# Performance work log

Hardware: AMD Instinct MI355X
Metric: run time of the kernel (lower is better)

## Reference

```python
import jax, jax.numpy as jnp
import numpy as np

B, S, D, E, K, FF = 4, 2048, 1024, 8, 2, 4096  # batch, seq, d_model, experts, top-k, 4*d_model


def setup_inputs() -> dict:
    key = jax.random.key(0)
    k0, k1, k2, k3 = jax.random.split(key, 4)
    scale = 0.02
    return {
        "x": jax.random.normal(k0, (B, S, D), jnp.float32),
        "gate_w": jax.random.normal(k1, (D, E), jnp.float32) * scale,
        "w1": jax.random.normal(k2, (E, D, FF), jnp.float32) * scale,
        "b1": jnp.zeros((E, FF), jnp.float32),
        "w2": jax.random.normal(k3, (E, FF, D), jnp.float32) * scale,
        "b2": jnp.zeros((E, D), jnp.float32),
    }


def reference(x, gate_w, w1, b1, w2, b2):
    # Gating: top-k logits, softmax over the selected k (matches torch.topk + softmax)
    logits = jnp.einsum("bsd,de->bse", x, gate_w)  # [B,S,E]
    vals, idxs = jax.lax.top_k(logits, K)           # [B,S,K]
    w = jax.nn.softmax(vals, axis=-1)               # [B,S,K]
    n_exp = gate_w.shape[-1]
    # Per-token combine weight for each expert (0 if not selected)
    combine = jnp.sum(jax.nn.one_hot(idxs, n_exp, dtype=x.dtype) * w[..., None], axis=-2)  # [B,S,E]

    out = jnp.zeros_like(x)
    for e in range(n_exp):  # fixed small loop over experts
        h = jax.nn.silu(jnp.einsum("bsd,df->bsf", x, w1[e]) + b1[e])  # dropout = identity (eval)
        y = jnp.einsum("bsf,fd->bsd", h, w2[e]) + b2[e]
        out = out + combine[..., e:e + 1] * y
    return out
```

## Files before the change

kernel.cpp:

```cpp
#include <hip/hip_runtime.h>
#include <math.h>

#define Tt 8192
#define Dd 1024
#define Ee 8
#define FFf 4096
#define SLOTS (Tt*2)

typedef unsigned short u16;
typedef unsigned int u32;
typedef __attribute__((ext_vector_type(8))) __bf16 bf16x8;
typedef __attribute__((ext_vector_type(4))) float f32x4;

__device__ __forceinline__ u16 f2bf(float f) {
  union { float f; u32 u; } v; v.f = f;
  u32 u = v.u;
  return (u16)((u + 0x7FFFu + ((u >> 16) & 1u)) >> 16);
}
__device__ __forceinline__ float bf2f(u16 h) {
  union { u32 u; float f; } v; v.u = ((u32)h) << 16; return v.f;
}
__device__ __forceinline__ void gl2lds16(const u16* g, u16* l) {
  __builtin_amdgcn_global_load_lds((const __attribute__((address_space(1))) void*)g,
                                   (__attribute__((address_space(3))) void*)l, 16, 0, 0);
}

__global__ void gate_topk_kernel(const float* __restrict__ x,
                                 const float* __restrict__ gw,
                                 int* __restrict__ counts,
                                 int* __restrict__ tok_e,
                                 float* __restrict__ tok_w,
                                 u16* __restrict__ xb) {
  int wave = (int)((blockIdx.x * blockDim.x + threadIdx.x) >> 6);
  int lane = threadIdx.x & 63;
  if (wave >= Tt) return;
  const float* xrow = x + (size_t)wave * Dd;
  int d0 = lane * 16;
  const f32x4* xr4 = (const f32x4*)(xrow + d0);
  f32x4 v0 = xr4[0], v1 = xr4[1], v2 = xr4[2], v3 = xr4[3];
  float xv[16];
#pragma unroll
  for (int k = 0; k < 4; k++) { xv[k] = v0[k]; xv[4 + k] = v1[k]; xv[8 + k] = v2[k]; xv[12 + k] = v3[k]; }
  float p[Ee];
#pragma unroll
  for (int e = 0; e < Ee; e++) p[e] = 0.f;
#pragma unroll
  for (int i = 0; i < 16; i++) {
    const float* g = gw + (size_t)(d0 + i) * Ee;
#pragma unroll
    for (int e = 0; e < Ee; e++) p[e] += xv[i] * g[e];
  }
  {
    uint4 o0, o1;
    o0.x = (u32)f2bf(xv[0]) | ((u32)f2bf(xv[1]) << 16);
    o0.y = (u32)f2bf(xv[2]) | ((u32)f2bf(xv[3]) << 16);
    o0.z = (u32)f2bf(xv[4]) | ((u32)f2bf(xv[5]) << 16);
    o0.w = (u32)f2bf(xv[6]) | ((u32)f2bf(xv[7]) << 16);
    o1.x = (u32)f2bf(xv[8]) | ((u32)f2bf(xv[9]) << 16);
    o1.y = (u32)f2bf(xv[10]) | ((u32)f2bf(xv[11]) << 16);
    o1.z = (u32)f2bf(xv[12]) | ((u32)f2bf(xv[13]) << 16);
    o1.w = (u32)f2bf(xv[14]) | ((u32)f2bf(xv[15]) << 16);
    u16* dp = xb + (size_t)wave * Dd + d0;
    *(uint4*)dp = o0;
    *(uint4*)(dp + 8) = o1;
  }
#pragma unroll
  for (int e = 0; e < Ee; e++) {
    for (int off = 32; off > 0; off >>= 1) p[e] += __shfl_xor(p[e], off, 64);
  }
  if (lane == 0) {
    int e0 = 0; float v0s = p[0];
#pragma unroll
    for (int e = 1; e < Ee; e++) if (p[e] > v0s) { v0s = p[e]; e0 = e; }
    int e1 = -1; float v1s = -INFINITY;
#pragma unroll
    for (int e = 0; e < Ee; e++) if (e != e0 && p[e] > v1s) { v1s = p[e]; e1 = e; }
    float w0 = 1.f / (1.f + expf(v1s - v0s));
    float w1 = 1.f - w0;
    tok_e[wave * 2 + 0] = e0; tok_e[wave * 2 + 1] = e1;
    tok_w[wave * 2 + 0] = w0; tok_w[wave * 2 + 1] = w1;
    atomicAdd(&counts[e0], 1);
    atomicAdd(&counts[e1], 1);
  }
}

__global__ __launch_bounds__(256) void wconv_kernel(const float* __restrict__ src,
                                                    u16* __restrict__ dst, int R, int C) {
  __shared__ float t[64][65];
  int e = blockIdx.z;
  size_t ebase = (size_t)e * R * C;
  int r0 = blockIdx.y * 64, c0 = blockIdx.x * 64;
  int tid = threadIdx.x;
  int row = tid >> 2, q = tid & 3;
  const float* sp = src + ebase + (size_t)(r0 + row) * C + c0 + q * 16;
  f32x4 v0 = *(const f32x4*)(sp);
  f32x4 v1 = *(const f32x4*)(sp + 4);
  f32x4 v2 = *(const f32x4*)(sp + 8);
  f32x4 v3 = *(const f32x4*)(sp + 12);
#pragma unroll
  for (int k = 0; k < 4; k++) t[row][q * 16 + k] = v0[k];
#pragma unroll
  for (int k = 0; k < 4; k++) t[row][q * 16 + 4 + k] = v1[k];
#pragma unroll
  for (int k = 0; k < 4; k++) t[row][q * 16 + 8 + k] = v2[k];
#pragma unroll
  for (int k = 0; k < 4; k++) t[row][q * 16 + 12 + k] = v3[k];
  __syncthreads();
  float c[16];
#pragma unroll
  for (int k = 0; k < 16; k++) c[k] = t[q * 16 + k][row];
  uint4 d0, d1;
  d0.x = (u32)f2bf(c[0]) | ((u32)f2bf(c[1]) << 16);
  d0.y = (u32)f2bf(c[2]) | ((u32)f2bf(c[3]) << 16);
  d0.z = (u32)f2bf(c[4]) | ((u32)f2bf(c[5]) << 16);
  d0.w = (u32)f2bf(c[6]) | ((u32)f2bf(c[7]) << 16);
  d1.x = (u32)f2bf(c[8]) | ((u32)f2bf(c[9]) << 16);
  d1.y = (u32)f2bf(c[10]) | ((u32)f2bf(c[11]) << 16);
  d1.z = (u32)f2bf(c[12]) | ((u32)f2bf(c[13]) << 16);
  d1.w = (u32)f2bf(c[14]) | ((u32)f2bf(c[15]) << 16);
  u16* dp = dst + ebase + (size_t)(c0 + row) * R + r0 + q * 16;
  *(uint4*)dp = d0;
  *(uint4*)(dp + 8) = d1;
}

__global__ void scan_kernel(const int* __restrict__ counts,
                            int* __restrict__ offsets, int* __restrict__ cursors) {
  if (threadIdx.x == 0 && blockIdx.x == 0) {
    int acc = 0;
    for (int e = 0; e < Ee; e++) { offsets[e] = acc; cursors[e] = acc; acc += counts[e]; }
  }
}

__global__ void scatter_kernel(const int* __restrict__ tok_e, const float* __restrict__ tok_w,
                               int* __restrict__ cursors,
                               int* __restrict__ slot_token, float* __restrict__ slot_w,
                               int* __restrict__ tok_slot) {
  int t = blockIdx.x * blockDim.x + threadIdx.x;
  if (t >= Tt) return;
#pragma unroll
  for (int k = 0; k < 2; k++) {
    int e = tok_e[t * 2 + k];
    int pos = atomicAdd(&cursors[e], 1);
    slot_token[pos] = t;
    slot_w[pos] = tok_w[t * 2 + k];
    tok_slot[t * 2 + k] = pos;
  }
}

#define MFMA16(H)                                                                 \
  do {                                                                            \
    acc[H][0][0] = __builtin_amdgcn_mfma_f32_16x16x32_bf16(a0, b0, acc[H][0][0], 0, 0, 0); \
    acc[H][0][1] = __builtin_amdgcn_mfma_f32_16x16x32_bf16(a0, b1, acc[H][0][1], 0, 0, 0); \
    acc[H][0][2] = __builtin_amdgcn_mfma_f32_16x16x32_bf16(a0, b2, acc[H][0][2], 0, 0, 0); \
    acc[H][0][3] = __builtin_amdgcn_mfma_f32_16x16x32_bf16(a0, b3, acc[H][0][3], 0, 0, 0); \
    acc[H][1][0] = __builtin_amdgcn_mfma_f32_16x16x32_bf16(a1, b0, acc[H][1][0], 0, 0, 0); \
    acc[H][1][1] = __builtin_amdgcn_mfma_f32_16x16x32_bf16(a1, b1, acc[H][1][1], 0, 0, 0); \
    acc[H][1][2] = __builtin_amdgcn_mfma_f32_16x16x32_bf16(a1, b2, acc[H][1][2], 0, 0, 0); \
    acc[H][1][3] = __builtin_amdgcn_mfma_f32_16x16x32_bf16(a1, b3, acc[H][1][3], 0, 0, 0); \
    acc[H][2][0] = __builtin_amdgcn_mfma_f32_16x16x32_bf16(a2, b0, acc[H][2][0], 0, 0, 0); \
    acc[H][2][1] = __builtin_amdgcn_mfma_f32_16x16x32_bf16(a2, b1, acc[H][2][1], 0, 0, 0); \
    acc[H][2][2] = __builtin_amdgcn_mfma_f32_16x16x32_bf16(a2, b2, acc[H][2][2], 0, 0, 0); \
    acc[H][2][3] = __builtin_amdgcn_mfma_f32_16x16x32_bf16(a2, b3, acc[H][2][3], 0, 0, 0); \
    acc[H][3][0] = __builtin_amdgcn_mfma_f32_16x16x32_bf16(a3, b0, acc[H][3][0], 0, 0, 0); \
    acc[H][3][1] = __builtin_amdgcn_mfma_f32_16x16x32_bf16(a3, b1, acc[H][3][1], 0, 0, 0); \
    acc[H][3][2] = __builtin_amdgcn_mfma_f32_16x16x32_bf16(a3, b2, acc[H][3][2], 0, 0, 0); \
    acc[H][3][3] = __builtin_amdgcn_mfma_f32_16x16x32_bf16(a3, b3, acc[H][3][3], 0, 0, 0); \
  } while (0)

template<int KDIM, int NDIM, int EPI, int GATHER, int NT>
__device__ __forceinline__ void moe_body(
    const u16* __restrict__ A, const u16* __restrict__ BT,
    const float* __restrict__ bias,
    const int* __restrict__ offsets, const int* __restrict__ counts,
    const int* __restrict__ slot_token, const float* __restrict__ slot_w,
    u16* __restrict__ O16, float* __restrict__ Of,
    int rb, int kbase) {
  int e = blockIdx.z;
  int cnt = counts[e];
  if (rb * 256 >= cnt) return;
  int off = offsets[e];
  int n0 = blockIdx.x * 256;

  __shared__ u16 S[65536];

  int tid = threadIdx.x;
  int lane = tid & 63, wave = tid >> 6;
  int wr = wave >> 2, wc = wave & 3;
  int lr = lane & 15, g = lane >> 4;

  const u16* BTe = BT + (size_t)e * NDIM * KDIM;

  const u16* aSrc[2][2];
  const u16* bSrc[2][2];
  int amax = off + cnt - 1;
#pragma unroll
  for (int h = 0; h < 2; h++)
#pragma unroll
    for (int s = 0; s < 2; s++) {
      int c = tid + s * 512;
      int lc = c ^ (((c >> 5) & 1) << 1);
      int ks = lc >> 9, rl = (lc >> 2) & 127, seg = lc & 3;
      int slotRow = off + rb * 256 + h * 128 + rl;
      if (slotRow > amax) slotRow = amax;
      int arow = GATHER ? slot_token[slotRow] : slotRow;
      aSrc[h][s] = A + (size_t)arow * KDIM + kbase + ks * 32 + seg * 8;
    }
#pragma unroll
  for (int ks = 0; ks < 2; ks++)
#pragma unroll
    for (int s = 0; s < 2; s++) {
      int c = tid + s * 512;
      int lc = c ^ (((c >> 5) & 1) << 1);
      int row = lc >> 2, seg = lc & 3;
      bSrc[ks][s] = BTe + (size_t)(n0 + row) * KDIM + kbase + ks * 32 + seg * 8;
    }

  auto stA = [&](int u, int h) {
    u16* d = &S[(u & 1) * 16384 + h * 8192 + wave * 512];
    gl2lds16(aSrc[h][0] + (size_t)u * 64, d);
    gl2lds16(aSrc[h][1] + (size_t)u * 64, d + 4096);
  };
  auto stB = [&](int u, int ks) {
    u16* d = &S[32768 + (u & 1) * 16384 + ks * 8192 + wave * 512];
    gl2lds16(bSrc[ks][0] + (size_t)u * 64, d);
    gl2lds16(bSrc[ks][1] + (size_t)u * 64, d + 4096);
  };
  auto rdA = [&](int dbuf, int hm, int ks, int i) -> bf16x8 {
    int rl = wr * 64 + i * 16 + lr;
    int logb = ks * 8192 + rl * 64 + g * 16;
    int phys = logb ^ (((rl >> 3) & 1) << 5);
    return *reinterpret_cast<const bf16x8*>(&S[dbuf * 16384 + hm * 8192 + (phys >> 1)]);
  };
  auto rdB = [&](int dbuf, int ks, int j) -> bf16x8 {
    int row = wc * 64 + j * 16 + lr;
    int logb = row * 64 + g * 16;
    int phys = logb ^ (((row >> 3) & 1) << 5);
    return *reinterpret_cast<const bf16x8*>(&S[32768 + dbuf * 16384 + ks * 8192 + (phys >> 1)]);
  };

  f32x4 acc[2][4][4];
#pragma unroll
  for (int h = 0; h < 2; h++)
#pragma unroll
    for (int i = 0; i < 4; i++)
#pragma unroll
      for (int j = 0; j < 4; j++) acc[h][i][j] = (f32x4)(0.0f);

  stB(0, 0); stA(0, 0); stA(0, 1); stB(0, 1);
  stB(1, 0); stA(1, 0);
  asm volatile("s_waitcnt vmcnt(4)" ::: "memory");
  __builtin_amdgcn_s_barrier();

  bf16x8 b0, b1, b2, b3;
  for (int t = 0; t < NT; ++t) {
    int dbuf = t & 1;
    {
      bf16x8 a0 = rdA(dbuf, 0, 0, 0), a1 = rdA(dbuf, 0, 0, 1),
             a2 = rdA(dbuf, 0, 0, 2), a3 = rdA(dbuf, 0, 0, 3);
      b0 = rdB(dbuf, 0, 0); b1 = rdB(dbuf, 0, 1); b2 = rdB(dbuf, 0, 2); b3 = rdB(dbuf, 0, 3);
      if (t + 1 < NT) stA(t + 1, 1);
      __builtin_amdgcn_s_barrier();
      asm volatile("s_waitcnt lgkmcnt(0)" ::: "memory");
      __builtin_amdgcn_sched_barrier(0);
      __builtin_amdgcn_s_setprio(1);
      MFMA16(0);
      __builtin_amdgcn_s_setprio(0);
      __builtin_amdgcn_s_barrier();
    }
    {
      bf16x8 a0 = rdA(dbuf, 1, 0, 0), a1 = rdA(dbuf, 1, 0, 1),
             a2 = rdA(dbuf, 1, 0, 2), a3 = rdA(dbuf, 1, 0, 3);
      if (t + 1 < NT) {
        stB(t + 1, 1);
        asm volatile("s_waitcnt vmcnt(6)" ::: "memory");
      }
      __builtin_amdgcn_s_barrier();
      asm volatile("s_waitcnt lgkmcnt(0)" ::: "memory");
      __builtin_amdgcn_sched_barrier(0);
      __builtin_amdgcn_s_setprio(1);
      MFMA16(1);
      __builtin_amdgcn_s_setprio(0);
      __builtin_amdgcn_s_barrier();
    }
    {
      bf16x8 a0 = rdA(dbuf, 0, 1, 0), a1 = rdA(dbuf, 0, 1, 1),
             a2 = rdA(dbuf, 0, 1, 2), a3 = rdA(dbuf, 0, 1, 3);
      b0 = rdB(dbuf, 1, 0); b1 = rdB(dbuf, 1, 1); b2 = rdB(dbuf, 1, 2); b3 = rdB(dbuf, 1, 3);
      if (t + 2 < NT) stB(t + 2, 0);
      __builtin_amdgcn_s_barrier();
      asm volatile("s_waitcnt lgkmcnt(0)" ::: "memory");
      __builtin_amdgcn_sched_barrier(0);
      __builtin_amdgcn_s_setprio(1);
      MFMA16(0);
      __builtin_amdgcn_s_setprio(0);
      __builtin_amdgcn_s_barrier();
    }
    {
      bf16x8 a0 = rdA(dbuf, 1, 1, 0), a1 = rdA(dbuf, 1, 1, 1),
             a2 = rdA(dbuf, 1, 1, 2), a3 = rdA(dbuf, 1, 1, 3);
      if (t + 2 < NT) {
        stA(t + 2, 0);
        asm volatile("s_waitcnt vmcnt(6)" ::: "memory");
      } else if (t + 1 < NT) {
        asm volatile("s_waitcnt vmcnt(0)" ::: "memory");
      }
      __builtin_amdgcn_s_barrier();
      asm volatile("s_waitcnt lgkmcnt(0)" ::: "memory");
      __builtin_amdgcn_sched_barrier(0);
      __builtin_amdgcn_s_setprio(1);
      MFMA16(1);
      __builtin_amdgcn_s_setprio(0);
      __builtin_amdgcn_s_barrier();
    }
  }

  int rlim = cnt - rb * 256;
#pragma unroll
  for (int hm = 0; hm < 2; hm++)
#pragma unroll
    for (int i = 0; i < 4; i++)
#pragma unroll
      for (int q = 0; q < 4; q++) {
        int m = hm * 128 + wr * 64 + i * 16 + g * 4 + q;
        if (m < rlim) {
          int slot = off + rb * 256 + m;
#pragma unroll
          for (int j = 0; j < 4; j++) {
            int n = n0 + wc * 64 + j * 16 + lr;
            float v = acc[hm][i][j][q];
            if (bias != nullptr) v += bias[e * NDIM + n];
            if (EPI == 0) {
              float sv = v / (1.f + expf(-v));
              O16[(size_t)slot * NDIM + n] = f2bf(sv);
            } else if (EPI == 1) {
              O16[(size_t)slot * NDIM + n] = f2bf(v * slot_w[slot]);
            } else {
              atomicAdd(Of + (size_t)slot_token[slot] * NDIM + n, v * slot_w[slot]);
            }
          }
        }
      }
}

__global__ __launch_bounds__(512, 2) void moe_g1_kernel(
    const u16* __restrict__ A, const u16* __restrict__ BT, const float* __restrict__ bias,
    const int* __restrict__ offsets, const int* __restrict__ counts,
    const int* __restrict__ slot_token, const float* __restrict__ slot_w,
    u16* __restrict__ O16) {
  moe_body<Dd, FFf, 0, 1, Dd / 64>(A, BT, bias, offsets, counts, slot_token, slot_w,
                                   O16, nullptr, blockIdx.y, 0);
}
__global__ __launch_bounds__(512, 2) void moe_g2s_kernel(
    const u16* __restrict__ A, const u16* __restrict__ BT, const float* __restrict__ bias,
    const int* __restrict__ offsets, const int* __restrict__ counts,
    const int* __restrict__ slot_token, const float* __restrict__ slot_w,
    u16* __restrict__ y) {
  int ksp = blockIdx.y & 1;
  moe_body<FFf, Dd, 1, 0, FFf / 128>(A, BT, ksp ? nullptr : bias, offsets, counts,
                                     slot_token, slot_w,
                                     y + (size_t)ksp * SLOTS * Dd, nullptr,
                                     blockIdx.y >> 1, ksp * (FFf / 2));
}
__global__ __launch_bounds__(512, 2) void moe_g2_kernel(
    const u16* __restrict__ A, const u16* __restrict__ BT, const float* __restrict__ bias,
    const int* __restrict__ offsets, const int* __restrict__ counts,
    const int* __restrict__ slot_token, const float* __restrict__ slot_w,
    u16* __restrict__ O16) {
  moe_body<FFf, Dd, 1, 0, FFf / 64>(A, BT, bias, offsets, counts, slot_token, slot_w,
                                    O16, nullptr, blockIdx.y, 0);
}
__global__ __launch_bounds__(512, 2) void moe_g2_atomic_kernel(
    const u16* __restrict__ A, const u16* __restrict__ BT, const float* __restrict__ bias,
    const int* __restrict__ offsets, const int* __restrict__ counts,
    const int* __restrict__ slot_token, const float* __restrict__ slot_w,
    float* __restrict__ Of) {
  moe_body<FFf, Dd, 2, 0, FFf / 64>(A, BT, bias, offsets, counts, slot_token, slot_w,
                                    nullptr, Of, blockIdx.y, 0);
}

__global__ void combine_kernel(const u16* __restrict__ y, const int* __restrict__ tok_slot,
                               float* __restrict__ out) {
  int gid = blockIdx.x * blockDim.x + threadIdx.x;
  int t = gid >> 7;
  int seg = gid & 127;
  int s0 = tok_slot[t * 2 + 0], s1 = tok_slot[t * 2 + 1];
  uint4 a = *(const uint4*)(y + (size_t)s0 * Dd + seg * 8);
  uint4 b = *(const uint4*)(y + (size_t)s1 * Dd + seg * 8);
  f32x4 o0, o1;
  o0[0] = bf2f((u16)a.x) + bf2f((u16)b.x);
  o0[1] = bf2f((u16)(a.x >> 16)) + bf2f((u16)(b.x >> 16));
  o0[2] = bf2f((u16)a.y) + bf2f((u16)b.y);
  o0[3] = bf2f((u16)(a.y >> 16)) + bf2f((u16)(b.y >> 16));
  o1[0] = bf2f((u16)a.z) + bf2f((u16)b.z);
  o1[1] = bf2f((u16)(a.z >> 16)) + bf2f((u16)(b.z >> 16));
  o1[2] = bf2f((u16)a.w) + bf2f((u16)b.w);
  o1[3] = bf2f((u16)(a.w >> 16)) + bf2f((u16)(b.w >> 16));
  float* op = out + (size_t)t * Dd + seg * 8;
  *(f32x4*)op = o0;
  *(f32x4*)(op + 4) = o1;
}

__global__ void combine4_kernel(const u16* __restrict__ y, const int* __restrict__ tok_slot,
                                float* __restrict__ out) {
  int gid = blockIdx.x * blockDim.x + threadIdx.x;
  int t = gid >> 7;
  int seg = gid & 127;
  int s0 = tok_slot[t * 2 + 0], s1 = tok_slot[t * 2 + 1];
  const u16* y1 = y + (size_t)SLOTS * Dd;
  uint4 a = *(const uint4*)(y  + (size_t)s0 * Dd + seg * 8);
  uint4 b = *(const uint4*)(y1 + (size_t)s0 * Dd + seg * 8);
  uint4 c = *(const uint4*)(y  + (size_t)s1 * Dd + seg * 8);
  uint4 d = *(const uint4*)(y1 + (size_t)s1 * Dd + seg * 8);
  f32x4 o0, o1;
  o0[0] = bf2f((u16)a.x) + bf2f((u16)b.x) + bf2f((u16)c.x) + bf2f((u16)d.x);
  o0[1] = bf2f((u16)(a.x >> 16)) + bf2f((u16)(b.x >> 16)) + bf2f((u16)(c.x >> 16)) + bf2f((u16)(d.x >> 16));
  o0[2] = bf2f((u16)a.y) + bf2f((u16)b.y) + bf2f((u16)c.y) + bf2f((u16)d.y);
  o0[3] = bf2f((u16)(a.y >> 16)) + bf2f((u16)(b.y >> 16)) + bf2f((u16)(c.y >> 16)) + bf2f((u16)(d.y >> 16));
  o1[0] = bf2f((u16)a.z) + bf2f((u16)b.z) + bf2f((u16)c.z) + bf2f((u16)d.z);
  o1[1] = bf2f((u16)(a.z >> 16)) + bf2f((u16)(b.z >> 16)) + bf2f((u16)(c.z >> 16)) + bf2f((u16)(d.z >> 16));
  o1[2] = bf2f((u16)a.w) + bf2f((u16)b.w) + bf2f((u16)c.w) + bf2f((u16)d.w);
  o1[3] = bf2f((u16)(a.w >> 16)) + bf2f((u16)(b.w >> 16)) + bf2f((u16)(c.w >> 16)) + bf2f((u16)(d.w >> 16));
  float* op = out + (size_t)t * Dd + seg * 8;
  *(f32x4*)op = o0;
  *(f32x4*)(op + 4) = o1;
}

extern "C" void kernel_launch(void* const* d_in, const int* in_sizes, int n_in,
                              void* d_out, int out_size, void* d_ws, size_t ws_size,
                              hipStream_t stream) {
  const float* x  = (const float*)d_in[0];
  const float* gw = (const float*)d_in[1];
  const float* w1 = (const float*)d_in[2];
  const float* b1 = (const float*)d_in[3];
  const float* w2 = (const float*)d_in[4];
  const float* b2 = (const float*)d_in[5];
  float* out = (float*)d_out;

  char* ws = (char*)d_ws;
  size_t off_counts = 0;
  size_t off_offsets = 256;
  size_t off_cursors = 512;
  size_t off_tok_e = 1024;
  size_t off_tok_w     = off_tok_e + (size_t)Tt * 2 * 4;
  size_t off_tok_slot  = off_tok_w + (size_t)Tt * 2 * 4;
  size_t off_slot_token= off_tok_slot + (size_t)Tt * 2 * 4;
  size_t off_slot_w    = off_slot_token + (size_t)SLOTS * 4;
  size_t off_xb        = off_slot_w + (size_t)SLOTS * 4;
  size_t off_h         = off_xb + (size_t)Tt * Dd * 2;
  size_t off_wT        = off_h + (size_t)SLOTS * FFf * 2;
  size_t off_y         = off_wT + (size_t)Ee * Dd * FFf * 2;
  size_t need_atomic   = off_y;
  size_t need_y1       = off_y + (size_t)SLOTS * Dd * 2;
  size_t need_y2       = off_y + (size_t)SLOTS * Dd * 2 * 2;
  if (ws_size < need_atomic) return;
  int tier = (ws_size >= need_y2) ? 2 : (ws_size >= need_y1) ? 1 : 0;

  int* counts     = (int*)(ws + off_counts);
  int* offsets    = (int*)(ws + off_offsets);
  int* cursors    = (int*)(ws + off_cursors);
  int* tok_e      = (int*)(ws + off_tok_e);
  float* tok_w    = (float*)(ws + off_tok_w);
  int* tok_slot   = (int*)(ws + off_tok_slot);
  int* slot_token = (int*)(ws + off_slot_token);
  float* slot_w   = (float*)(ws + off_slot_w);
  u16* xb         = (u16*)(ws + off_xb);
  u16* h          = (u16*)(ws + off_h);
  u16* wT         = (u16*)(ws + off_wT);
  u16* y          = (u16*)(ws + off_y);

  hipMemsetAsync(ws, 0, 1024, stream);

  gate_topk_kernel<<<Tt / 4, 256, 0, stream>>>(x, gw, counts, tok_e, tok_w, xb);
  scan_kernel<<<1, 64, 0, stream>>>(counts, offsets, cursors);
  scatter_kernel<<<Tt / 256, 256, 0, stream>>>(tok_e, tok_w, cursors, slot_token, slot_w, tok_slot);

  {
    dim3 gc(FFf / 64, Dd / 64, Ee);
    wconv_kernel<<<gc, 256, 0, stream>>>(w1, wT, Dd, FFf);
  }
  {
    dim3 g1(FFf / 256, Tt / 256, Ee);
    moe_g1_kernel<<<g1, 512, 0, stream>>>(xb, wT, b1, offsets, counts,
                                          slot_token, slot_w, h);
  }
  {
    dim3 gc(Dd / 64, FFf / 64, Ee);
    wconv_kernel<<<gc, 256, 0, stream>>>(w2, wT, FFf, Dd);
  }
  if (tier == 2) {
    dim3 g2(Dd / 256, (Tt / 256) * 2, Ee);
    moe_g2s_kernel<<<g2, 512, 0, stream>>>(h, wT, b2, offsets, counts,
                                           slot_token, slot_w, y);
    combine4_kernel<<<(Tt * 128) / 256, 256, 0, stream>>>(y, tok_slot, out);
  } else if (tier == 1) {
    dim3 g2(Dd / 256, Tt / 256, Ee);
    moe_g2_kernel<<<g2, 512, 0, stream>>>(h, wT, b2, offsets, counts,
                                          slot_token, slot_w, y);
    combine_kernel<<<(Tt * 128) / 256, 256, 0, stream>>>(y, tok_slot, out);
  } else {
    hipMemsetAsync(d_out, 0, (size_t)out_size * sizeof(float), stream);
    dim3 g2(Dd / 256, Tt / 256, Ee);
    moe_g2_atomic_kernel<<<g2, 512, 0, stream>>>(h, wT, b2, offsets, counts,
                                                 slot_token, slot_w, out);
  }
}
```

Before: 848.5 us.

## Fold scan into gating kernel, recoalesce weight transpose, unroll GEMM loop

The single-thread scan kernel is removed and its offsets/cursors computation is done by the last block of the gating kernel, detected with a done counter and threadfence. The weight transpose-and-convert kernel is reorganised so each thread loads one float4 per row and writes 8-element bf16 chunks, giving more coalesced global access. The main GEMM K-loop gets an unroll-by-2 pragma. These save a kernel launch and aim to speed up weight conversion, at the cost of an extra atomic per block and possibly higher register use in the GEMM.

```diff
diff --git a/kernel.cpp b/kernel.cpp
--- a/kernel.cpp
+++ b/kernel.cpp
@@ -30,10 +30,12 @@
                                  int* __restrict__ counts,
                                  int* __restrict__ tok_e,
                                  float* __restrict__ tok_w,
-                                 u16* __restrict__ xb) {
+                                 u16* __restrict__ xb,
+                                 int* __restrict__ offsets,
+                                 int* __restrict__ cursors,
+                                 int* __restrict__ done) {
   int wave = (int)((blockIdx.x * blockDim.x + threadIdx.x) >> 6);
   int lane = threadIdx.x & 63;
-  if (wave >= Tt) return;
   const float* xrow = x + (size_t)wave * Dd;
   int d0 = lane * 16;
   const f32x4* xr4 = (const f32x4*)(xrow + d0);
@@ -82,6 +84,15 @@
     atomicAdd(&counts[e0], 1);
     atomicAdd(&counts[e1], 1);
   }
+  __syncthreads();
+  if (threadIdx.x == 0) {
+    __threadfence();
+    int t = atomicAdd(done, 1);
+    if (t == (int)gridDim.x - 1) {
+      int acc = 0;
+      for (int e = 0; e < Ee; e++) { offsets[e] = acc; cursors[e] = acc; acc += counts[e]; }
+    }
+  }
 }
 
 __global__ __launch_bounds__(256) void wconv_kernel(const float* __restrict__ src,
@@ -91,43 +102,29 @@
   size_t ebase = (size_t)e * R * C;
   int r0 = blockIdx.y * 64, c0 = blockIdx.x * 64;
   int tid = threadIdx.x;
-  int row = tid >> 2, q = tid & 3;
-  const float* sp = src + ebase + (size_t)(r0 + row) * C + c0 + q * 16;
-  f32x4 v0 = *(const f32x4*)(sp);
-  f32x4 v1 = *(const f32x4*)(sp + 4);
-  f32x4 v2 = *(const f32x4*)(sp + 8);
-  f32x4 v3 = *(const f32x4*)(sp + 12);
-#pragma unroll
-  for (int k = 0; k < 4; k++) t[row][q * 16 + k] = v0[k];
-#pragma unroll
-  for (int k = 0; k < 4; k++) t[row][q * 16 + 4 + k] = v1[k];
-#pragma unroll
-  for (int k = 0; k < 4; k++) t[row][q * 16 + 8 + k] = v2[k];
-#pragma unroll
-  for (int k = 0; k < 4; k++) t[row][q * 16 + 12 + k] = v3[k];
+  int rr = tid >> 4;
+  int cc = (tid & 15) * 4;
+#pragma unroll
+  for (int p = 0; p < 4; p++) {
+    int row = rr + p * 16;
+    f32x4 v = *(const f32x4*)(src + ebase + (size_t)(r0 + row) * C + c0 + cc);
+    t[row][cc] = v[0]; t[row][cc + 1] = v[1]; t[row][cc + 2] = v[2]; t[row][cc + 3] = v[3];
+  }
   __syncthreads();
-  float c[16];
-#pragma unroll
-  for (int k = 0; k < 16; k++) c[k] = t[q * 16 + k][row];
-  uint4 d0, d1;
-  d0.x = (u32)f2bf(c[0]) | ((u32)f2bf(c[1]) << 16);
-  d0.y = (u32)f2bf(c[2]) | ((u32)f2bf(c[3]) << 16);
-  d0.z = (u32)f2bf(c[4]) | ((u32)f2bf(c[5]) << 16);
-  d0.w = (u32)f2bf(c[6]) | ((u32)f2bf(c[7]) << 16);
-  d1.x = (u32)f2bf(c[8]) | ((u32)f2bf(c[9]) << 16);
-  d1.y = (u32)f2bf(c[10]) | ((u32)f2bf(c[11]) << 16);
-  d1.z = (u32)f2bf(c[12]) | ((u32)f2bf(c[13]) << 16);
-  d1.w = (u32)f2bf(c[14]) | ((u32)f2bf(c[15]) << 16);
-  u16* dp = dst + ebase + (size_t)(c0 + row) * R + r0 + q * 16;
-  *(uint4*)dp = d0;
-  *(uint4*)(dp + 8) = d1;
-}
-
-__global__ void scan_kernel(const int* __restrict__ counts,
-                            int* __restrict__ offsets, int* __restrict__ cursors) {
-  if (threadIdx.x == 0 && blockIdx.x == 0) {
-    int acc = 0;
-    for (int e = 0; e < Ee; e++) { offsets[e] = acc; cursors[e] = acc; acc += counts[e]; }
+  int c = tid >> 3;
+  int rseg = (tid & 7) * 8;
+#pragma unroll
+  for (int p = 0; p < 2; p++) {
+    int cp = c + p * 32;
+    float f[8];
+#pragma unroll
+    for (int i = 0; i < 8; i++) f[i] = t[rseg + i][cp];
+    uint4 o;
+    o.x = (u32)f2bf(f[0]) | ((u32)f2bf(f[1]) << 16);
+    o.y = (u32)f2bf(f[2]) | ((u32)f2bf(f[3]) << 16);
+    o.z = (u32)f2bf(f[4]) | ((u32)f2bf(f[5]) << 16);
+    o.w = (u32)f2bf(f[6]) | ((u32)f2bf(f[7]) << 16);
+    *(uint4*)(dst + ebase + (size_t)(c0 + cp) * R + r0 + rseg) = o;
   }
 }
 
@@ -252,6 +249,7 @@
   __builtin_amdgcn_s_barrier();
 
   bf16x8 b0, b1, b2, b3;
+#pragma unroll 2
   for (int t = 0; t < NT; ++t) {
     int dbuf = t & 1;
     {
@@ -359,7 +357,7 @@
   moe_body<FFf, Dd, 1, 0, FFf / 128>(A, BT, ksp ? nullptr : bias, offsets, counts,
                                      slot_token, slot_w,
                                      y + (size_t)ksp * SLOTS * Dd, nullptr,
-                                     blockIdx.y >> 1, ksp * (FFf / 2));
+                                     (int)(blockIdx.y >> 1), ksp * (FFf / 2));
 }
 __global__ __launch_bounds__(512, 2) void moe_g2_kernel(
     const u16* __restrict__ A, const u16* __restrict__ BT, const float* __restrict__ bias,
@@ -440,6 +438,7 @@
   size_t off_counts = 0;
   size_t off_offsets = 256;
   size_t off_cursors = 512;
+  size_t off_done = 768;
   size_t off_tok_e = 1024;
   size_t off_tok_w     = off_tok_e + (size_t)Tt * 2 * 4;
   size_t off_tok_slot  = off_tok_w + (size_t)Tt * 2 * 4;
@@ -458,6 +457,7 @@
   int* counts     = (int*)(ws + off_counts);
   int* offsets    = (int*)(ws + off_offsets);
   int* cursors    = (int*)(ws + off_cursors);
+  int* done       = (int*)(ws + off_done);
   int* tok_e      = (int*)(ws + off_tok_e);
   float* tok_w    = (float*)(ws + off_tok_w);
   int* tok_slot   = (int*)(ws + off_tok_slot);
@@ -470,8 +470,8 @@
 
   hipMemsetAsync(ws, 0, 1024, stream);
 
-  gate_topk_kernel<<<Tt / 4, 256, 0, stream>>>(x, gw, counts, tok_e, tok_w, xb);
-  scan_kernel<<<1, 64, 0, stream>>>(counts, offsets, cursors);
+  gate_topk_kernel<<<Tt / 4, 256, 0, stream>>>(x, gw, counts, tok_e, tok_w, xb,
+                                               offsets, cursors, done);
   scatter_kernel<<<Tt / 256, 256, 0, stream>>>(tok_e, tok_w, cursors, slot_token, slot_w, tok_slot);
 
   {
```

Result: no change. 851.1 us (+0.3%).
